# Kernel tuning notes

Measured on AMD Instinct MI355X. Metric: run time of the kernel, lower is better.

The kernel has to match this reference:

```python
import jax, jax.numpy as jnp
import numpy as np

NUM_NODES, MEM_DIM, MSG_DIM, TIME_DIM = 65536, 128, 128, 128
POS_DIM = MEM_DIM  # PositionMessage reshape forces pos_embedding_dim == memory_dim
IN_MEM = MSG_DIM + 2 * MEM_DIM + TIME_DIM  # IdentityMessage width = 512
IN_POS = POS_DIM + 2 * MEM_DIM + TIME_DIM  # PositionMessage width = 512


def setup_inputs() -> dict:
    key = jax.random.key(0)
    ks = jax.random.split(key, 24)
    s = jnp.float32(0.05)
    f = lambda k, sh: jax.random.normal(k, sh, jnp.float32)
    return dict(
        n_id=jnp.arange(NUM_NODES, dtype=jnp.int32),
        memory=f(ks[0], (NUM_NODES, MEM_DIM)),
        pos_mem=f(ks[1], (NUM_NODES, MEM_DIM)),
        pos_emb=f(ks[2], (NUM_NODES, POS_DIM)),
        raw_msg_s=f(ks[3], (NUM_NODES, MSG_DIM)),
        raw_msg_d=f(ks[4], (NUM_NODES, MSG_DIM)),
        other_s=jax.random.randint(ks[5], (NUM_NODES,), 0, NUM_NODES, jnp.int32),
        other_d=jax.random.randint(ks[6], (NUM_NODES,), 0, NUM_NODES, jnp.int32),
        t_s=jax.random.randint(ks[7], (NUM_NODES,), 1000, 2000, jnp.int32),
        t_d=jax.random.randint(ks[8], (NUM_NODES,), 1000, 2000, jnp.int32),
        last_update=jax.random.randint(ks[9], (NUM_NODES,), 0, 1000, jnp.int32),
        w_time_mem=f(ks[10], (TIME_DIM,)) * s, b_time_mem=f(ks[11], (TIME_DIM,)) * s,
        w_time_pos=f(ks[12], (TIME_DIM,)) * s, b_time_pos=f(ks[13], (TIME_DIM,)) * s,
        Wih_mem=f(ks[14], (3 * MEM_DIM, IN_MEM)) * s, Whh_mem=f(ks[15], (3 * MEM_DIM, MEM_DIM)) * s,
        bih_mem=f(ks[16], (3 * MEM_DIM,)) * s, bhh_mem=f(ks[17], (3 * MEM_DIM,)) * s,
        Wih_pos=f(ks[18], (3 * MEM_DIM, IN_POS)) * s, Whh_pos=f(ks[19], (3 * MEM_DIM, MEM_DIM)) * s,
        bih_pos=f(ks[20], (3 * MEM_DIM,)) * s, bhh_pos=f(ks[21], (3 * MEM_DIM,)) * s,
    )


def _time_enc(t_rel, w, b):
    # PyG TimeEncoder: cos(Linear(1, time_dim)(t_rel))
    return jnp.cos(t_rel[:, None] * w[None, :] + b[None, :])


def _gru(x, h, Wih, Whh, bih, bhh):
    # torch.nn.GRUCell math
    gi = x @ Wih.T + bih
    gh = h @ Whh.T + bhh
    ir, iz, inn = jnp.split(gi, 3, axis=-1)
    hr, hz, hn = jnp.split(gh, 3, axis=-1)
    r = jax.nn.sigmoid(ir + hr)
    z = jax.nn.sigmoid(iz + hz)
    n = jnp.tanh(inn + r * hn)
    return (1.0 - z) * n + z * h


def _tgn_memory(mem, n_id, other_s, other_d, feat_s, feat_d, t_s, t_d,
                last_update, w_t, b_t, Wih, Whh, bih, bhh):
    # Gather per-node state; each node owns one src-store and one dst-store message.
    h = mem[n_id]                                        # [N, D]
    lu = last_update[n_id].astype(jnp.float32)
    te_s = _time_enc(t_s.astype(jnp.float32) - lu, w_t, b_t)
    te_d = _time_enc(t_d.astype(jnp.float32) - lu, w_t, b_t)
    msg_s = jnp.concatenate([h, mem[other_s], feat_s, te_s], axis=-1)  # [N, IN]
    msg_d = jnp.concatenate([h, mem[other_d], feat_d, te_d], axis=-1)
    # LastAggregator: keep the most recent message per node (scatter_max on t)
    pick_s = (t_s >= t_d)[:, None]
    aggr = jnp.where(pick_s, msg_s, msg_d)
    z = _gru(aggr, h, Wih, Whh, bih, bhh)
    new_lu = jnp.maximum(t_s, t_d)
    return z, new_lu


def reference(n_id, memory, pos_mem, pos_emb, raw_msg_s, raw_msg_d,
              other_s, other_d, t_s, t_d, last_update,
              w_time_mem, b_time_mem, w_time_pos, b_time_pos,
              Wih_mem, Whh_mem, bih_mem, bhh_mem,
              Wih_pos, Whh_pos, bih_pos, bhh_pos):
    z, last_up = _tgn_memory(memory, n_id, other_s, other_d, raw_msg_s, raw_msg_d,
                             t_s, t_d, last_update,
                             w_time_mem, b_time_mem, Wih_mem, Whh_mem, bih_mem, bhh_mem)
    # pos raw message is the event's src node id -> embedding lookup
    pos_z, _ = _tgn_memory(pos_mem, n_id, other_s, other_d,
                           pos_emb[n_id], pos_emb[other_d],
                           t_s, t_d, last_update,
                           w_time_pos, b_time_pos, Wih_pos, Whh_pos, bih_pos, bhh_pos)
    return z, pos_z, last_up
```

## Files before the change

### kernel.cpp

```cpp
#include <hip/hip_runtime.h>
#include <hip/hip_bf16.h>
#include <math.h>

#define NODES   65536
#define DD      128
#define BM      64
#define BK      32
#define NST     16
#define NWT     20
#define NSUB    24
#define WTILE_STRIDE (NSUB * 64 * 8)
#define WG_STRIDE    (NWT * WTILE_STRIDE)

typedef __bf16 bf16x8 __attribute__((ext_vector_type(8)));
typedef float  f32x4  __attribute__((ext_vector_type(4)));

static __device__ __forceinline__ unsigned short f2bf(float f) {
    __hip_bfloat16 h = __float2bfloat16(f);
    return *reinterpret_cast<unsigned short*>(&h);
}
static __device__ __forceinline__ float sigmoidf_(float x) {
    return 1.0f / (1.0f + __expf(-x));
}

__global__ void prep_w_kernel(const float* __restrict__ Wih0, const float* __restrict__ Whh0,
                              const float* __restrict__ Wih1, const float* __restrict__ Whh1,
                              unsigned short* __restrict__ Wws) {
    int gid = blockIdx.x * 256 + threadIdx.x;
    if (gid >= 2 * WG_STRIDE) return;
    int g   = gid / WG_STRIDE;
    int r   = gid - g * WG_STRIDE;
    int kt  = r / WTILE_STRIDE;
    int r2  = r - kt * WTILE_STRIDE;
    int t   = r2 >> 9;
    int l8  = r2 & 511;
    int lane = l8 >> 3, j = l8 & 7;
    int cl  = lane & 15, q = lane >> 4;
    int n   = t * 16 + cl;
    const float* Wih = g ? Wih1 : Wih0;
    const float* Whh = g ? Whh1 : Whh0;
    float v;
    if (kt < 16) v = Wih[n * 512 + kt * 32 + q * 8 + j];
    else         v = Whh[n * 128 + (kt - 16) * 32 + q * 8 + j];
    Wws[gid] = f2bf(v);
}

__global__ __launch_bounds__(512, 4) void tgn_fused_kernel(
    const int*   __restrict__ n_id,
    const float* __restrict__ memory_,
    const float* __restrict__ pos_mem,
    const float* __restrict__ pos_emb,
    const float* __restrict__ raw_s,
    const float* __restrict__ raw_d,
    const int*   __restrict__ other_s,
    const int*   __restrict__ other_d,
    const int*   __restrict__ t_s,
    const int*   __restrict__ t_d,
    const int*   __restrict__ last_update,
    const float* __restrict__ w_time_mem, const float* __restrict__ b_time_mem,
    const float* __restrict__ w_time_pos, const float* __restrict__ b_time_pos,
    const float* __restrict__ bih_mem, const float* __restrict__ bhh_mem,
    const float* __restrict__ bih_pos, const float* __restrict__ bhh_pos,
    const unsigned short* __restrict__ Wws,
    float* __restrict__ out)
{
    __shared__ __align__(16) unsigned short Xls[2][BM * BK];
    __shared__ int   snid[BM];
    __shared__ int   soth[BM];
    __shared__ float sdt[BM];
    __shared__ int   sfeat[BM];

    const int g   = blockIdx.y;
    const int nb  = blockIdx.x;
    const int tid = threadIdx.x;

    const float* mem_g = g ? pos_mem    : memory_;
    const float* wt    = g ? w_time_pos : w_time_mem;
    const float* bt    = g ? b_time_pos : b_time_mem;
    const float* bih   = g ? bih_pos    : bih_mem;
    const float* bhh   = g ? bhh_pos    : bhh_mem;

    if (tid < BM) {
        int gi   = nb * BM + tid;
        int id   = n_id[gi];
        int ts   = t_s[gi];
        int td   = t_d[gi];
        bool pick = (ts >= td);
        int oth  = pick ? other_s[gi] : other_d[gi];
        int lu   = last_update[id];
        float dt = (float)(pick ? ts : td) - (float)lu;
        int code;
        if (g) code = pick ? id : other_d[gi];
        else   code = pick ? gi : ~gi;
        snid[tid]  = id;
        soth[tid]  = oth;
        sdt[tid]   = dt;
        sfeat[tid] = code;
        if (g == 0) {
            out[2 * (size_t)NODES * DD + gi] = (float)max(ts, td);
        }
    }

    f32x4 acc[16];
    #pragma unroll
    for (int i = 0; i < 16; ++i) acc[i] = (f32x4){0.f, 0.f, 0.f, 0.f};

    const int lane = tid & 63;
    const int wave = tid >> 6;
    const int wm   = wave & 1;
    const int wd   = wave >> 1;
    const int m0   = wm * 32;
    const int d0   = wd * 32;
    const int q    = lane >> 4;
    const int cl   = lane & 15;

    const int si = tid >> 3;
    const int sc = (tid & 7) * 4;

    const unsigned short* wbase = Wws + (size_t)g * WG_STRIDE + lane * 8;
    const int tR = 2 * wd;
    const int tZ = 8 + 2 * wd;
    const int tN = 16 + 2 * wd;

    #define MFMA(s, tc, a, b) \
        acc[((s)) * 2 + (tc)] = __builtin_amdgcn_mfma_f32_16x16x32_bf16((a), (b), acc[((s)) * 2 + (tc)], 0, 0, 0); \
        acc[(4 + (s)) * 2 + (tc)] = __builtin_amdgcn_mfma_f32_16x16x32_bf16((a1), (b), acc[(4 + (s)) * 2 + (tc)], 0, 0, 0);

    auto stageX = [&](int st, unsigned short* buf) {
        int seg = st >> 2;
        int col = (st & 3) * 32 + sc;
        float4 v;
        if (seg == 3) {
            float dt = sdt[si];
            float4 wv = *(const float4*)(wt + col);
            float4 bv = *(const float4*)(bt + col);
            v.x = cosf(dt * wv.x + bv.x);
            v.y = cosf(dt * wv.y + bv.y);
            v.z = cosf(dt * wv.z + bv.z);
            v.w = cosf(dt * wv.w + bv.w);
        } else {
            const float* src;
            if (seg == 0)            src = mem_g + (size_t)snid[si] * DD + col;
            else if (seg == 1)       src = mem_g + (size_t)soth[si] * DD + col;
            else {
                int code = sfeat[si];
                if (g)               src = pos_emb + (size_t)code * DD + col;
                else if (code >= 0)  src = raw_s + (size_t)code * DD + col;
                else                 src = raw_d + (size_t)(~code) * DD + col;
            }
            v = *(const float4*)src;
        }
        ushort4 pv;
        pv.x = f2bf(v.x); pv.y = f2bf(v.y); pv.z = f2bf(v.z); pv.w = f2bf(v.w);
        *(ushort4*)(buf + si * BK + sc) = pv;
    };

    __syncthreads();
    stageX(0, Xls[0]);
    __syncthreads();

    for (int st = 0; st < NST; ++st) {
        unsigned short* cur = Xls[st & 1];
        bf16x8 a0 = *(const bf16x8*)(cur + (m0 + cl) * BK + q * 8);
        bf16x8 a1 = *(const bf16x8*)(cur + (m0 + 16 + cl) * BK + q * 8);
        if (st < NST - 1) stageX(st + 1, Xls[(st + 1) & 1]);
        __syncthreads();

        const unsigned short* wk = wbase + (size_t)st * WTILE_STRIDE;
        bf16x8 bR0 = *(const bf16x8*)(wk + (tR    ) * 512);
        bf16x8 bR1 = *(const bf16x8*)(wk + (tR + 1) * 512);
        bf16x8 bZ0 = *(const bf16x8*)(wk + (tZ    ) * 512);
        bf16x8 bZ1 = *(const bf16x8*)(wk + (tZ + 1) * 512);
        bf16x8 bN0 = *(const bf16x8*)(wk + (tN    ) * 512);
        bf16x8 bN1 = *(const bf16x8*)(wk + (tN + 1) * 512);
        MFMA(0, 0, a0, bR0)  MFMA(0, 1, a0, bR1)
        MFMA(1, 0, a0, bZ0)  MFMA(1, 1, a0, bZ1)
        MFMA(2, 0, a0, bN0)  MFMA(2, 1, a0, bN1)

        if (st < 4) {
            const unsigned short* wh = wbase + (size_t)(16 + st) * WTILE_STRIDE;
            bf16x8 cR0 = *(const bf16x8*)(wh + (tR    ) * 512);
            bf16x8 cR1 = *(const bf16x8*)(wh + (tR + 1) * 512);
            bf16x8 cZ0 = *(const bf16x8*)(wh + (tZ    ) * 512);
            bf16x8 cZ1 = *(const bf16x8*)(wh + (tZ + 1) * 512);
            bf16x8 cN0 = *(const bf16x8*)(wh + (tN    ) * 512);
            bf16x8 cN1 = *(const bf16x8*)(wh + (tN + 1) * 512);
            MFMA(0, 0, a0, cR0)  MFMA(0, 1, a0, cR1)
            MFMA(1, 0, a0, cZ0)  MFMA(1, 1, a0, cZ1)
            MFMA(3, 0, a0, cN0)  MFMA(3, 1, a0, cN1)
        }
    }
    #undef MFMA

    float* outz = out + (size_t)g * NODES * DD;
    #pragma unroll
    for (int tc = 0; tc < 2; ++tc) {
        int d = d0 + tc * 16 + cl;
        float br  = bih[d]       + bhh[d];
        float bz  = bih[128 + d] + bhh[128 + d];
        float bni = bih[256 + d];
        float bnh = bhh[256 + d];
        #pragma unroll
        for (int am = 0; am < 2; ++am) {
            #pragma unroll
            for (int r = 0; r < 4; ++r) {
                int il = m0 + am * 16 + q * 4 + r;
                float rs  = acc[(am * 4 + 0) * 2 + tc][r] + br;
                float zs  = acc[(am * 4 + 1) * 2 + tc][r] + bz;
                float in_ = acc[(am * 4 + 2) * 2 + tc][r] + bni;
                float hn_ = acc[(am * 4 + 3) * 2 + tc][r] + bnh;
                float rg = sigmoidf_(rs);
                float zg = sigmoidf_(zs);
                float nv = tanhf(in_ + rg * hn_);
                float h  = mem_g[(size_t)snid[il] * DD + d];
                outz[(size_t)(nb * BM + il) * DD + d] = (1.0f - zg) * nv + zg * h;
            }
        }
    }
}

extern "C" void kernel_launch(void* const* d_in, const int* in_sizes, int n_in,
                              void* d_out, int out_size, void* d_ws, size_t ws_size,
                              hipStream_t stream) {
    const int*   n_id        = (const int*)  d_in[0];
    const float* memory_     = (const float*)d_in[1];
    const float* pos_mem     = (const float*)d_in[2];
    const float* pos_emb     = (const float*)d_in[3];
    const float* raw_s       = (const float*)d_in[4];
    const float* raw_d       = (const float*)d_in[5];
    const int*   other_s     = (const int*)  d_in[6];
    const int*   other_d     = (const int*)  d_in[7];
    const int*   t_s         = (const int*)  d_in[8];
    const int*   t_d         = (const int*)  d_in[9];
    const int*   last_update = (const int*)  d_in[10];
    const float* w_time_mem  = (const float*)d_in[11];
    const float* b_time_mem  = (const float*)d_in[12];
    const float* w_time_pos  = (const float*)d_in[13];
    const float* b_time_pos  = (const float*)d_in[14];
    const float* Wih_mem     = (const float*)d_in[15];
    const float* Whh_mem     = (const float*)d_in[16];
    const float* bih_mem     = (const float*)d_in[17];
    const float* bhh_mem     = (const float*)d_in[18];
    const float* Wih_pos     = (const float*)d_in[19];
    const float* Whh_pos     = (const float*)d_in[20];
    const float* bih_pos     = (const float*)d_in[21];
    const float* bhh_pos     = (const float*)d_in[22];

    unsigned short* Wws = (unsigned short*)d_ws;
    float* out = (float*)d_out;

    prep_w_kernel<<<(2 * WG_STRIDE + 255) / 256, 256, 0, stream>>>(
        Wih_mem, Whh_mem, Wih_pos, Whh_pos, Wws);

    dim3 grid(NODES / BM, 2);
    tgn_fused_kernel<<<grid, 512, 0, stream>>>(
        n_id, memory_, pos_mem, pos_emb, raw_s, raw_d,
        other_s, other_d, t_s, t_d, last_update,
        w_time_mem, b_time_mem, w_time_pos, b_time_pos,
        bih_mem, bhh_mem, bih_pos, bhh_pos,
        Wws, out);
}
```

Before: 347.2 us.

## Stage full input row tile in LDS once and remap waves to column tiles

Replaces the per-K-step double-buffered staging with a single up-front gather of the whole 64x512 bf16 input tile into LDS (with a padded row stride), done by waves split by segment. The barrier inside the K loop goes away, and each wave now owns one 16-column tile across all 64 rows, so it loads half as many weight fragments per step while reading more A fragments. It also swaps in fast cos (range-reduced hardware cos), exp-based tanh and bit-trick bf16 rounding. In exchange the LDS footprint grows to about 70KB, which can limit occupancy, the gather no longer overlaps with MFMA work, and the fast math is less accurate.

```diff
diff --git a/kernel.cpp b/kernel.cpp
--- a/kernel.cpp
+++ b/kernel.cpp
@@ -5,22 +5,32 @@
 #define NODES   65536
 #define DD      128
 #define BM      64
-#define BK      32
 #define NST     16
-#define NWT     20
 #define NSUB    24
 #define WTILE_STRIDE (NSUB * 64 * 8)
-#define WG_STRIDE    (NWT * WTILE_STRIDE)
+#define WG_STRIDE    (20 * WTILE_STRIDE)
+#define XW      544
 
 typedef __bf16 bf16x8 __attribute__((ext_vector_type(8)));
 typedef float  f32x4  __attribute__((ext_vector_type(4)));
 
 static __device__ __forceinline__ unsigned short f2bf(float f) {
-    __hip_bfloat16 h = __float2bfloat16(f);
-    return *reinterpret_cast<unsigned short*>(&h);
-}
-static __device__ __forceinline__ float sigmoidf_(float x) {
+    union { float f; unsigned u; } v; v.f = f;
+    return (unsigned short)((v.u + 0x8000u) >> 16);
+}
+static __device__ __forceinline__ float fastcos(float x) {
+    float r = x * 0.15915494309189535f;
+    r = r - floorf(r);
+    return __builtin_amdgcn_cosf(r);
+}
+static __device__ __forceinline__ float fsigmoid(float x) {
     return 1.0f / (1.0f + __expf(-x));
+}
+static __device__ __forceinline__ float ftanh(float x) {
+    float ax = fabsf(x);
+    float t  = __expf(-2.0f * ax);
+    float th = 1.0f - 2.0f * t / (1.0f + t);
+    return copysignf(th, x);
 }
 
 __global__ void prep_w_kernel(const float* __restrict__ Wih0, const float* __restrict__ Whh0,
@@ -64,7 +74,7 @@
     const unsigned short* __restrict__ Wws,
     float* __restrict__ out)
 {
-    __shared__ __align__(16) unsigned short Xls[2][BM * BK];
+    __shared__ __align__(16) unsigned short X[BM * XW];
     __shared__ int   snid[BM];
     __shared__ int   soth[BM];
     __shared__ float sdt[BM];
@@ -73,6 +83,8 @@
     const int g   = blockIdx.y;
     const int nb  = blockIdx.x;
     const int tid = threadIdx.x;
+    const int lane = tid & 63;
+    const int wave = tid >> 6;
 
     const float* mem_g = g ? pos_mem    : memory_;
     const float* wt    = g ? w_time_pos : w_time_mem;
@@ -100,121 +112,108 @@
             out[2 * (size_t)NODES * DD + gi] = (float)max(ts, td);
         }
     }
+    __syncthreads();
+
+    {
+        int row = lane;
+        if (wave >= 6) {
+            float dt = sdt[row];
+            int c0 = (wave - 6) * 64;
+            #pragma unroll
+            for (int i = 0; i < 16; ++i) {
+                int c = c0 + i * 4;
+                float4 wv = *(const float4*)(wt + c);
+                float4 bv = *(const float4*)(bt + c);
+                ushort4 pv;
+                pv.x = f2bf(fastcos(dt * wv.x + bv.x));
+                pv.y = f2bf(fastcos(dt * wv.y + bv.y));
+                pv.z = f2bf(fastcos(dt * wv.z + bv.z));
+                pv.w = f2bf(fastcos(dt * wv.w + bv.w));
+                *(ushort4*)(X + row * XW + 384 + c) = pv;
+            }
+        } else {
+            int seg = wave >> 1;
+            int c0  = (wave & 1) * 64;
+            const float* src;
+            if (seg == 0)      src = mem_g + (size_t)snid[row] * DD + c0;
+            else if (seg == 1) src = mem_g + (size_t)soth[row] * DD + c0;
+            else {
+                int code = sfeat[row];
+                if (g)              src = pos_emb + (size_t)code * DD + c0;
+                else if (code >= 0) src = raw_s + (size_t)code * DD + c0;
+                else                src = raw_d + (size_t)(~code) * DD + c0;
+            }
+            #pragma unroll
+            for (int i = 0; i < 16; ++i) {
+                float4 v = *(const float4*)(src + i * 4);
+                ushort4 pv;
+                pv.x = f2bf(v.x); pv.y = f2bf(v.y); pv.z = f2bf(v.z); pv.w = f2bf(v.w);
+                *(ushort4*)(X + row * XW + seg * 128 + c0 + i * 4) = pv;
+            }
+        }
+    }
+    __syncthreads();
 
     f32x4 acc[16];
     #pragma unroll
     for (int i = 0; i < 16; ++i) acc[i] = (f32x4){0.f, 0.f, 0.f, 0.f};
 
-    const int lane = tid & 63;
-    const int wave = tid >> 6;
-    const int wm   = wave & 1;
-    const int wd   = wave >> 1;
-    const int m0   = wm * 32;
-    const int d0   = wd * 32;
-    const int q    = lane >> 4;
-    const int cl   = lane & 15;
-
-    const int si = tid >> 3;
-    const int sc = (tid & 7) * 4;
-
+    const int q  = lane >> 4;
+    const int cl = lane & 15;
     const unsigned short* wbase = Wws + (size_t)g * WG_STRIDE + lane * 8;
-    const int tR = 2 * wd;
-    const int tZ = 8 + 2 * wd;
-    const int tN = 16 + 2 * wd;
-
-    #define MFMA(s, tc, a, b) \
-        acc[((s)) * 2 + (tc)] = __builtin_amdgcn_mfma_f32_16x16x32_bf16((a), (b), acc[((s)) * 2 + (tc)], 0, 0, 0); \
-        acc[(4 + (s)) * 2 + (tc)] = __builtin_amdgcn_mfma_f32_16x16x32_bf16((a1), (b), acc[(4 + (s)) * 2 + (tc)], 0, 0, 0);
-
-    auto stageX = [&](int st, unsigned short* buf) {
-        int seg = st >> 2;
-        int col = (st & 3) * 32 + sc;
-        float4 v;
-        if (seg == 3) {
-            float dt = sdt[si];
-            float4 wv = *(const float4*)(wt + col);
-            float4 bv = *(const float4*)(bt + col);
-            v.x = cosf(dt * wv.x + bv.x);
-            v.y = cosf(dt * wv.y + bv.y);
-            v.z = cosf(dt * wv.z + bv.z);
-            v.w = cosf(dt * wv.w + bv.w);
-        } else {
-            const float* src;
-            if (seg == 0)            src = mem_g + (size_t)snid[si] * DD + col;
-            else if (seg == 1)       src = mem_g + (size_t)soth[si] * DD + col;
-            else {
-                int code = sfeat[si];
-                if (g)               src = pos_emb + (size_t)code * DD + col;
-                else if (code >= 0)  src = raw_s + (size_t)code * DD + col;
-                else                 src = raw_d + (size_t)(~code) * DD + col;
-            }
-            v = *(const float4*)src;
-        }
-        ushort4 pv;
-        pv.x = f2bf(v.x); pv.y = f2bf(v.y); pv.z = f2bf(v.z); pv.w = f2bf(v.w);
-        *(ushort4*)(buf + si * BK + sc) = pv;
-    };
-
-    __syncthreads();
-    stageX(0, Xls[0]);
-    __syncthreads();
-
+    const int tR = wave, tZ = 8 + wave, tN = 16 + wave;
+
+    #pragma unroll
     for (int st = 0; st < NST; ++st) {
-        unsigned short* cur = Xls[st & 1];
-        bf16x8 a0 = *(const bf16x8*)(cur + (m0 + cl) * BK + q * 8);
-        bf16x8 a1 = *(const bf16x8*)(cur + (m0 + 16 + cl) * BK + q * 8);
-        if (st < NST - 1) stageX(st + 1, Xls[(st + 1) & 1]);
-        __syncthreads();
+        bf16x8 a[4];
+        #pragma unroll
+        for (int j = 0; j < 4; ++j)
+            a[j] = *(const bf16x8*)(X + (j * 16 + cl) * XW + st * 32 + q * 8);
 
         const unsigned short* wk = wbase + (size_t)st * WTILE_STRIDE;
-        bf16x8 bR0 = *(const bf16x8*)(wk + (tR    ) * 512);
-        bf16x8 bR1 = *(const bf16x8*)(wk + (tR + 1) * 512);
-        bf16x8 bZ0 = *(const bf16x8*)(wk + (tZ    ) * 512);
-        bf16x8 bZ1 = *(const bf16x8*)(wk + (tZ + 1) * 512);
-        bf16x8 bN0 = *(const bf16x8*)(wk + (tN    ) * 512);
-        bf16x8 bN1 = *(const bf16x8*)(wk + (tN + 1) * 512);
-        MFMA(0, 0, a0, bR0)  MFMA(0, 1, a0, bR1)
-        MFMA(1, 0, a0, bZ0)  MFMA(1, 1, a0, bZ1)
-        MFMA(2, 0, a0, bN0)  MFMA(2, 1, a0, bN1)
-
+        bf16x8 bR = *(const bf16x8*)(wk + tR * 512);
+        bf16x8 bZ = *(const bf16x8*)(wk + tZ * 512);
+        bf16x8 bN = *(const bf16x8*)(wk + tN * 512);
+        #pragma unroll
+        for (int j = 0; j < 4; ++j) {
+            acc[j * 4 + 0] = __builtin_amdgcn_mfma_f32_16x16x32_bf16(a[j], bR, acc[j * 4 + 0], 0, 0, 0);
+            acc[j * 4 + 1] = __builtin_amdgcn_mfma_f32_16x16x32_bf16(a[j], bZ, acc[j * 4 + 1], 0, 0, 0);
+            acc[j * 4 + 2] = __builtin_amdgcn_mfma_f32_16x16x32_bf16(a[j], bN, acc[j * 4 + 2], 0, 0, 0);
+        }
         if (st < 4) {
             const unsigned short* wh = wbase + (size_t)(16 + st) * WTILE_STRIDE;
-            bf16x8 cR0 = *(const bf16x8*)(wh + (tR    ) * 512);
-            bf16x8 cR1 = *(const bf16x8*)(wh + (tR + 1) * 512);
-            bf16x8 cZ0 = *(const bf16x8*)(wh + (tZ    ) * 512);
-            bf16x8 cZ1 = *(const bf16x8*)(wh + (tZ + 1) * 512);
-            bf16x8 cN0 = *(const bf16x8*)(wh + (tN    ) * 512);
-            bf16x8 cN1 = *(const bf16x8*)(wh + (tN + 1) * 512);
-            MFMA(0, 0, a0, cR0)  MFMA(0, 1, a0, cR1)
-            MFMA(1, 0, a0, cZ0)  MFMA(1, 1, a0, cZ1)
-            MFMA(3, 0, a0, cN0)  MFMA(3, 1, a0, cN1)
-        }
-    }
-    #undef MFMA
+            bf16x8 cR = *(const bf16x8*)(wh + tR * 512);
+            bf16x8 cZ = *(const bf16x8*)(wh + tZ * 512);
+            bf16x8 cN = *(const bf16x8*)(wh + tN * 512);
+            #pragma unroll
+            for (int j = 0; j < 4; ++j) {
+                acc[j * 4 + 0] = __builtin_amdgcn_mfma_f32_16x16x32_bf16(a[j], cR, acc[j * 4 + 0], 0, 0, 0);
+                acc[j * 4 + 1] = __builtin_amdgcn_mfma_f32_16x16x32_bf16(a[j], cZ, acc[j * 4 + 1], 0, 0, 0);
+                acc[j * 4 + 3] = __builtin_amdgcn_mfma_f32_16x16x32_bf16(a[j], cN, acc[j * 4 + 3], 0, 0, 0);
+            }
+        }
+    }
 
     float* outz = out + (size_t)g * NODES * DD;
+    const int d = wave * 16 + cl;
+    float br  = bih[d]       + bhh[d];
+    float bz  = bih[128 + d] + bhh[128 + d];
+    float bni = bih[256 + d];
+    float bnh = bhh[256 + d];
     #pragma unroll
-    for (int tc = 0; tc < 2; ++tc) {
-        int d = d0 + tc * 16 + cl;
-        float br  = bih[d]       + bhh[d];
-        float bz  = bih[128 + d] + bhh[128 + d];
-        float bni = bih[256 + d];
-        float bnh = bhh[256 + d];
+    for (int j = 0; j < 4; ++j) {
         #pragma unroll
-        for (int am = 0; am < 2; ++am) {
-            #pragma unroll
-            for (int r = 0; r < 4; ++r) {
-                int il = m0 + am * 16 + q * 4 + r;
-                float rs  = acc[(am * 4 + 0) * 2 + tc][r] + br;
-                float zs  = acc[(am * 4 + 1) * 2 + tc][r] + bz;
-                float in_ = acc[(am * 4 + 2) * 2 + tc][r] + bni;
-                float hn_ = acc[(am * 4 + 3) * 2 + tc][r] + bnh;
-                float rg = sigmoidf_(rs);
-                float zg = sigmoidf_(zs);
-                float nv = tanhf(in_ + rg * hn_);
-                float h  = mem_g[(size_t)snid[il] * DD + d];
-                outz[(size_t)(nb * BM + il) * DD + d] = (1.0f - zg) * nv + zg * h;
-            }
+        for (int r = 0; r < 4; ++r) {
+            int il = j * 16 + q * 4 + r;
+            float rs  = acc[j * 4 + 0][r] + br;
+            float zs  = acc[j * 4 + 1][r] + bz;
+            float in_ = acc[j * 4 + 2][r] + bni;
+            float hn_ = acc[j * 4 + 3][r] + bnh;
+            float rg = fsigmoid(rs);
+            float zg = fsigmoid(zs);
+            float nv = ftanh(in_ + rg * hn_);
+            float h  = mem_g[(size_t)snid[il] * DD + d];
+            outz[(size_t)(nb * BM + il) * DD + d] = (1.0f - zg) * nv + zg * h;
         }
     }
 }
```

Result: faster. 311.1 us (-10.4%).
